# Performance work log

Measured on AMD Instinct MI355X. Metric: run time of the kernel, lower is better.

Reference implementation:

```python
import jax, jax.numpy as jnp
import numpy as np

N_NODES = 100000
N_EDGES = 1600000
DIM = 32

def setup_inputs() -> dict:
    key = jax.random.key(0)
    k1, k2, k3, k4 = jax.random.split(key, 4)
    A_rows = jax.random.randint(k1, (N_EDGES,), 0, N_NODES, dtype=jnp.int32)
    A_cols = jax.random.randint(k2, (N_EDGES,), 0, N_NODES, dtype=jnp.int32)
    A_vals = jax.random.uniform(k3, (N_EDGES,), dtype=jnp.float32)
    x = jax.random.normal(k4, (N_NODES, DIM), dtype=jnp.float32)
    return {"A_rows": A_rows, "A_cols": A_cols, "A_vals": A_vals, "x": x}

def reference(A_rows, A_cols, A_vals, x):
    # SpMM: out[i] = sum_{e: rows[e]==i} vals[e] * x[cols[e]]
    # gather neighbor features along edges, scale by edge weight, scatter-add to rows
    msgs = A_vals[:, None] * x[A_cols]              # [E, d]
    out = jax.ops.segment_sum(msgs, A_rows, num_segments=x.shape[0])  # [n, d]
    return out
```

## Files before the change

### kernel.cpp

```cpp
#include <hip/hip_runtime.h>


#define N_NODES 100000
#define N_EDGES 1600000
#define DIM 32

#define CBR    256
#define NBC    ((N_NODES + CBR - 1) / CBR)
#define CHUNK  8
#define CAPC   6656
#define OCAP   16384

#define SC_BLOCKS   500
#define SC_THREADS  512
#define EPB         3200
#define EPT         7

#define SG_THREADS  1024
#define SG_EPT      7

#define OFF_GCNT    64
#define OFF_OVER    (OFF_GCNT + NBC * 64)
#define OFF_REGION  (((OFF_OVER + OCAP * 16) + 255) & ~255)
#define WS_NEEDED   ((size_t)OFF_REGION + (size_t)NBC * CAPC * 8)

__global__ __launch_bounds__(256) void spmm_atomic_kernel(
    const int* __restrict__ rows,
    const int* __restrict__ cols,
    const float* __restrict__ vals,
    const float* __restrict__ x,
    float* __restrict__ out)
{
    const long long idx = (long long)blockIdx.x * blockDim.x + threadIdx.x;
    const long long total = (long long)N_EDGES * DIM;
    if (idx >= total) return;

    const int e = (int)(idx >> 5);
    const int d = (int)(idx & 31);

    const int r   = rows[e];
    const int c   = cols[e];
    const float v = vals[e];

    const float xv = x[(long long)c * DIM + d];
    atomicAdd(&out[(long long)r * DIM + d], v * xv);
}

__global__ __launch_bounds__(SC_THREADS) void spmm_scatter_ws(
    const int* __restrict__ rows,
    const int* __restrict__ cols,
    const float* __restrict__ vals,
    int* __restrict__ gcnt,
    int2* __restrict__ region,
    int* __restrict__ ocount,
    int4* __restrict__ overflow)
{
    __shared__ int2 stage[EPB];
    __shared__ int  hist[NBC];
    __shared__ int  lstart[NBC];
    __shared__ int  gbase[NBC];
    __shared__ int  wsum[8];

    const int tid   = threadIdx.x;
    const int ebase = blockIdx.x * EPB;

    if (tid < NBC) hist[tid] = 0;
    __syncthreads();

    int en_x[EPT], en_y[EPT], eb[EPT], rk[EPT];
    #pragma unroll
    for (int i = 0; i < EPT; ++i) {
        const int o = i * SC_THREADS + tid;
        if (o < EPB) {
            const int e = ebase + o;
            const int r = rows[e];
            eb[i]   = r >> 8;
            en_x[i] = ((r & 255) << 17) | cols[e];
            en_y[i] = __float_as_int(vals[e]);
            rk[i]   = atomicAdd(&hist[eb[i]], 1);
        } else {
            eb[i] = -1; en_x[i] = 0; en_y[i] = 0; rk[i] = 0;
        }
    }
    __syncthreads();

    const int lane = tid & 63;
    const int wv   = tid >> 6;
    const int myh  = (tid < NBC) ? hist[tid] : 0;
    int s = myh;
    #pragma unroll
    for (int off = 1; off < 64; off <<= 1) {
        const int t = __shfl_up(s, off, 64);
        if (lane >= off) s += t;
    }
    if (lane == 63) wsum[wv] = s;
    __syncthreads();
    if (wv == 0) {
        const int t = (lane < 8) ? wsum[lane] : 0;
        int ss = t;
        #pragma unroll
        for (int off = 1; off < 8; off <<= 1) {
            const int u = __shfl_up(ss, off, 64);
            if (lane >= off) ss += u;
        }
        if (lane < 8) wsum[lane] = ss - t;
    }
    __syncthreads();
    if (tid < NBC) {
        lstart[tid] = s + wsum[wv] - myh;
        const int pad = (myh + 7) & ~7;
        gbase[tid] = pad ? atomicAdd(&gcnt[tid * 16], pad) : 0;
    }
    __syncthreads();

    #pragma unroll
    for (int i = 0; i < EPT; ++i) {
        if (eb[i] >= 0)
            stage[lstart[eb[i]] + rk[i]] = make_int2(en_x[i], en_y[i]);
    }
    __syncthreads();

    for (int bc = tid; bc < NBC; bc += SC_THREADS) {
        const int n   = hist[bc];
        const int ls  = lstart[bc];
        const int gb  = gbase[bc];
        const int nch = (n + 7) >> 3;
        for (int jch = 0; jch < nch; ++jch) {
            const int gpos = gb + jch * CHUNK;
            if (gpos + CHUNK <= CAPC) {
                int2* dst = region + (size_t)bc * CAPC + gpos;
                #pragma unroll
                for (int j = 0; j < CHUNK; ++j) {
                    const int k = jch * CHUNK + j;
                    dst[j] = (k < n) ? stage[ls + k] : make_int2(-1, 0);
                }
            } else {
                for (int j = 0; j < CHUNK; ++j) {
                    const int k = jch * CHUNK + j;
                    if (k < n) {
                        const int2 t = stage[ls + k];
                        const int op = atomicAdd(ocount, 1);
                        if (op < OCAP)
                            overflow[op] = make_int4((bc << 8) | (t.x >> 17),
                                                     t.x & 0x1FFFF, t.y, 0);
                    }
                }
            }
        }
    }
}

__global__ __launch_bounds__(SG_THREADS) void spmm_sort_gather(
    const int* __restrict__ gcnt,
    const int2* __restrict__ region,
    const int* __restrict__ ocount,
    const int4* __restrict__ overflow,
    const float* __restrict__ x,
    float* __restrict__ out)
{
    __shared__ int2 srt[CAPC];
    __shared__ int  hist[CBR];
    __shared__ int  startx[CBR];
    __shared__ int  excl_s[CBR];
    __shared__ int  wsum[4];

    const int bc  = blockIdx.x;
    const int tid = threadIdx.x;

    int n = gcnt[bc * 16]; if (n > CAPC) n = CAPC;
    const int2* __restrict__ slice = region + (size_t)bc * CAPC;

    if (tid < CBR) hist[tid] = 0;
    __syncthreads();

    int ex[SG_EPT], ey[SG_EPT], rk[SG_EPT];
    #pragma unroll
    for (int i = 0; i < SG_EPT; ++i) {
        const int k = i * SG_THREADS + tid;
        ex[i] = -1; ey[i] = 0; rk[i] = 0;
        if (k < n) {
            const int2 e = slice[k];
            ex[i] = e.x; ey[i] = e.y;
            if (e.x >= 0) rk[i] = atomicAdd(&hist[e.x >> 17], 1);
        }
    }
    __syncthreads();

    const int lane = tid & 63;
    const int wv   = tid >> 6;
    int h = 0, incl = 0;
    if (tid < CBR) {
        h = hist[tid];
        int s = h;
        #pragma unroll
        for (int off = 1; off < 64; off <<= 1) {
            const int t = __shfl_up(s, off, 64);
            if (lane >= off) s += t;
        }
        incl = s;
        if (lane == 63) wsum[wv] = s;
    }
    __syncthreads();
    if (wv == 0) {
        const int t = (lane < 4) ? wsum[lane] : 0;
        int ss = t;
        #pragma unroll
        for (int off = 1; off < 4; off <<= 1) {
            const int u = __shfl_up(ss, off, 64);
            if (lane >= off) ss += u;
        }
        if (lane < 4) wsum[lane] = ss - t;
    }
    __syncthreads();
    if (tid < CBR) {
        incl += wsum[wv];
        startx[tid] = incl;
        excl_s[tid] = incl - h;
    }
    __syncthreads();

    #pragma unroll
    for (int i = 0; i < SG_EPT; ++i) {
        if (ex[i] >= 0)
            srt[excl_s[ex[i] >> 17] + rk[i]] = make_int2(ex[i] & 0x1FFFF, ey[i]);
    }
    __syncthreads();

    const int wid = tid >> 6;
    const int eg  = lane >> 3;
    const int d4  = lane & 7;

    #pragma unroll
    for (int i = 0; i < 16; ++i) {
        const int lrow = wid * 16 + i;
        const int cnt  = hist[lrow];
        const int st   = startx[lrow] - cnt;

        float4 acc = make_float4(0.f, 0.f, 0.f, 0.f);
        for (int k0 = 0; k0 < cnt; k0 += 16) {
            const int ka = k0 + eg;
            const int kb = ka + 8;
            const int2 ea = (ka < cnt) ? srt[st + ka] : make_int2(0, 0);
            const int2 eb = (kb < cnt) ? srt[st + kb] : make_int2(0, 0);
            const float va = __int_as_float(ea.y);
            const float vb = __int_as_float(eb.y);
            const float4 xa = *(const float4*)&x[ea.x * DIM + d4 * 4];
            const float4 xb = *(const float4*)&x[eb.x * DIM + d4 * 4];
            acc.x = fmaf(va, xa.x, acc.x);  acc.y = fmaf(va, xa.y, acc.y);
            acc.z = fmaf(va, xa.z, acc.z);  acc.w = fmaf(va, xa.w, acc.w);
            acc.x = fmaf(vb, xb.x, acc.x);  acc.y = fmaf(vb, xb.y, acc.y);
            acc.z = fmaf(vb, xb.z, acc.z);  acc.w = fmaf(vb, xb.w, acc.w);
        }

        #pragma unroll
        for (int m = 8; m < 64; m <<= 1) {
            acc.x += __shfl_xor(acc.x, m, 64);
            acc.y += __shfl_xor(acc.y, m, 64);
            acc.z += __shfl_xor(acc.z, m, 64);
            acc.w += __shfl_xor(acc.w, m, 64);
        }

        const int r = bc * CBR + lrow;
        if (eg == 0 && r < N_NODES)
            *(float4*)&out[r * DIM + d4 * 4] = acc;
    }

    __syncthreads();
    int on = *ocount;
    if (on > 0) {
        if (on > OCAP) on = OCAP;
        for (int k = tid; k < on; k += SG_THREADS) {
            const int4 t = overflow[k];
            if ((t.x >> 8) == bc) {
                const float v = __int_as_float(t.z);
                const float* __restrict__ xr = x + (long long)t.y * DIM;
                float* orow = out + (long long)t.x * DIM;
                for (int d = 0; d < DIM; ++d)
                    atomicAdd(&orow[d], v * xr[d]);
            }
        }
    }
}

extern "C" void kernel_launch(void* const* d_in, const int* in_sizes, int n_in,
                              void* d_out, int out_size, void* d_ws, size_t ws_size,
                              hipStream_t stream) {
    const int*   A_rows = (const int*)d_in[0];
    const int*   A_cols = (const int*)d_in[1];
    const float* A_vals = (const float*)d_in[2];
    const float* x      = (const float*)d_in[3];
    float*       out    = (float*)d_out;

    if (d_ws == nullptr || ws_size < WS_NEEDED) {
        hipMemsetAsync(out, 0, (size_t)out_size * sizeof(float), stream);
        const long long total = (long long)N_EDGES * DIM;
        const int block = 256;
        const long long grid = (total + block - 1) / block;
        spmm_atomic_kernel<<<(dim3)(unsigned)grid, block, 0, stream>>>(
            A_rows, A_cols, A_vals, x, out);
        return;
    }

    char* ws = (char*)d_ws;
    int*  ocount   = (int*)ws;
    int*  gcnt     = (int*)(ws + OFF_GCNT);
    int4* overflow = (int4*)(ws + OFF_OVER);
    int2* region   = (int2*)(ws + OFF_REGION);

    hipMemsetAsync(ws, 0, OFF_OVER, stream);

    spmm_scatter_ws<<<SC_BLOCKS, SC_THREADS, 0, stream>>>(
        A_rows, A_cols, A_vals, gcnt, region, ocount, overflow);

    spmm_sort_gather<<<NBC, SG_THREADS, 0, stream>>>(
        gcnt, region, ocount, overflow, x, out);
}
```

Measured before the change: 132.3 us.

## Fuse memset, scatter and sort-gather into one cooperative kernel with grid syncs

```diff
diff --git a/kernel.cpp b/kernel.cpp
--- a/kernel.cpp
+++ b/kernel.cpp
@@ -1,4 +1,7 @@
 #include <hip/hip_runtime.h>
+#include <hip/hip_cooperative_groups.h>
+
+namespace cg = cooperative_groups;
 
 
 #define N_NODES 100000
@@ -11,13 +14,15 @@
 #define CAPC   6656
 #define OCAP   16384
 
+#define FB_THREADS 1024
+#define EPB1       4093
+#define EPT1       4
+#define EPT2       7
+
 #define SC_BLOCKS   500
 #define SC_THREADS  512
 #define EPB         3200
 #define EPT         7
-
-#define SG_THREADS  1024
-#define SG_EPT      7
 
 #define OFF_GCNT    64
 #define OFF_OVER    (OFF_GCNT + NBC * 64)
@@ -34,111 +39,117 @@
     const long long idx = (long long)blockIdx.x * blockDim.x + threadIdx.x;
     const long long total = (long long)N_EDGES * DIM;
     if (idx >= total) return;
-
     const int e = (int)(idx >> 5);
     const int d = (int)(idx & 31);
-
     const int r   = rows[e];
     const int c   = cols[e];
     const float v = vals[e];
-
-    const float xv = x[(long long)c * DIM + d];
-    atomicAdd(&out[(long long)r * DIM + d], v * xv);
+    atomicAdd(&out[(long long)r * DIM + d], v * x[(long long)c * DIM + d]);
 }
 
-__global__ __launch_bounds__(SC_THREADS) void spmm_scatter_ws(
+__global__ __launch_bounds__(FB_THREADS, 8) void spmm_fused(
     const int* __restrict__ rows,
     const int* __restrict__ cols,
     const float* __restrict__ vals,
     int* __restrict__ gcnt,
     int2* __restrict__ region,
     int* __restrict__ ocount,
-    int4* __restrict__ overflow)
+    int4* __restrict__ overflow,
+    const float* __restrict__ x,
+    float* __restrict__ out)
 {
-    __shared__ int2 stage[EPB];
+    __shared__ int2 buf[CAPC];
     __shared__ int  hist[NBC];
-    __shared__ int  lstart[NBC];
-    __shared__ int  gbase[NBC];
-    __shared__ int  wsum[8];
-
-    const int tid   = threadIdx.x;
-    const int ebase = blockIdx.x * EPB;
+    __shared__ int  aux1[NBC];
+    __shared__ int  aux2[NBC];
+    __shared__ int  wsum[16];
+
+    const int tid  = threadIdx.x;
+    const int bid  = blockIdx.x;
+    const int lane = tid & 63;
+    const int wv   = tid >> 6;
+    cg::grid_group grid = cg::this_grid();
+
+    for (int i = bid * FB_THREADS + tid; i < NBC * 16; i += NBC * FB_THREADS)
+        gcnt[i] = 0;
+    if (bid == 0 && tid == 0) *ocount = 0;
+    grid.sync();
 
     if (tid < NBC) hist[tid] = 0;
     __syncthreads();
 
-    int en_x[EPT], en_y[EPT], eb[EPT], rk[EPT];
-    #pragma unroll
-    for (int i = 0; i < EPT; ++i) {
-        const int o = i * SC_THREADS + tid;
-        if (o < EPB) {
-            const int e = ebase + o;
+    const int ebase = bid * EPB1;
+    int en_x[EPT1], en_y[EPT1], eb[EPT1], rk[EPT1];
+    #pragma unroll
+    for (int i = 0; i < EPT1; ++i) {
+        const int o = i * FB_THREADS + tid;
+        const int e = ebase + o;
+        eb[i] = -1; en_x[i] = 0; en_y[i] = 0; rk[i] = 0;
+        if (o < EPB1 && e < N_EDGES) {
             const int r = rows[e];
             eb[i]   = r >> 8;
             en_x[i] = ((r & 255) << 17) | cols[e];
             en_y[i] = __float_as_int(vals[e]);
             rk[i]   = atomicAdd(&hist[eb[i]], 1);
-        } else {
-            eb[i] = -1; en_x[i] = 0; en_y[i] = 0; rk[i] = 0;
-        }
-    }
-    __syncthreads();
-
-    const int lane = tid & 63;
-    const int wv   = tid >> 6;
-    const int myh  = (tid < NBC) ? hist[tid] : 0;
-    int s = myh;
-    #pragma unroll
-    for (int off = 1; off < 64; off <<= 1) {
-        const int t = __shfl_up(s, off, 64);
-        if (lane >= off) s += t;
-    }
-    if (lane == 63) wsum[wv] = s;
-    __syncthreads();
-    if (wv == 0) {
-        const int t = (lane < 8) ? wsum[lane] : 0;
-        int ss = t;
-        #pragma unroll
-        for (int off = 1; off < 8; off <<= 1) {
-            const int u = __shfl_up(ss, off, 64);
-            if (lane >= off) ss += u;
-        }
-        if (lane < 8) wsum[lane] = ss - t;
-    }
-    __syncthreads();
-    if (tid < NBC) {
-        lstart[tid] = s + wsum[wv] - myh;
-        const int pad = (myh + 7) & ~7;
-        gbase[tid] = pad ? atomicAdd(&gcnt[tid * 16], pad) : 0;
-    }
-    __syncthreads();
-
-    #pragma unroll
-    for (int i = 0; i < EPT; ++i) {
+        }
+    }
+    __syncthreads();
+
+    {
+        const int myh = (tid < NBC) ? hist[tid] : 0;
+        int s = myh;
+        #pragma unroll
+        for (int off = 1; off < 64; off <<= 1) {
+            const int t = __shfl_up(s, off, 64);
+            if (lane >= off) s += t;
+        }
+        if (lane == 63) wsum[wv] = s;
+        __syncthreads();
+        if (wv == 0) {
+            const int t = (lane < 16) ? wsum[lane] : 0;
+            int ss = t;
+            #pragma unroll
+            for (int off = 1; off < 16; off <<= 1) {
+                const int u = __shfl_up(ss, off, 64);
+                if (lane >= off) ss += u;
+            }
+            if (lane < 16) wsum[lane] = ss - t;
+        }
+        __syncthreads();
+        if (tid < NBC) {
+            aux1[tid] = s + wsum[wv] - myh;
+            const int pad = (myh + 7) & ~7;
+            aux2[tid] = pad ? atomicAdd(&gcnt[tid * 16], pad) : 0;
+        }
+    }
+    __syncthreads();
+
+    #pragma unroll
+    for (int i = 0; i < EPT1; ++i) {
         if (eb[i] >= 0)
-            stage[lstart[eb[i]] + rk[i]] = make_int2(en_x[i], en_y[i]);
-    }
-    __syncthreads();
-
-    for (int bc = tid; bc < NBC; bc += SC_THREADS) {
-        const int n   = hist[bc];
-        const int ls  = lstart[bc];
-        const int gb  = gbase[bc];
+            buf[aux1[eb[i]] + rk[i]] = make_int2(en_x[i], en_y[i]);
+    }
+    __syncthreads();
+
+    for (int bc = tid; bc < NBC; bc += FB_THREADS) {
+        const int n  = hist[bc];
+        const int ls = aux1[bc];
+        const int gb = aux2[bc];
         const int nch = (n + 7) >> 3;
-        for (int jch = 0; jch < nch; ++jch) {
-            const int gpos = gb + jch * CHUNK;
+        for (int j = 0; j < nch; ++j) {
+            const int gpos = gb + j * CHUNK;
             if (gpos + CHUNK <= CAPC) {
                 int2* dst = region + (size_t)bc * CAPC + gpos;
                 #pragma unroll
-                for (int j = 0; j < CHUNK; ++j) {
-                    const int k = jch * CHUNK + j;
-                    dst[j] = (k < n) ? stage[ls + k] : make_int2(-1, 0);
+                for (int q = 0; q < CHUNK; ++q) {
+                    const int k = j * CHUNK + q;
+                    dst[q] = (k < n) ? buf[ls + k] : make_int2(-1, 0);
                 }
             } else {
-                for (int j = 0; j < CHUNK; ++j) {
-                    const int k = jch * CHUNK + j;
+                for (int q = 0; q < CHUNK; ++q) {
+                    const int k = j * CHUNK + q;
                     if (k < n) {
-                        const int2 t = stage[ls + k];
+                        const int2 t = buf[ls + k];
                         const int op = atomicAdd(ocount, 1);
                         if (op < OCAP)
                             overflow[op] = make_int4((bc << 8) | (t.x >> 17),
@@ -148,46 +159,29 @@
             }
         }
     }
-}
-
-__global__ __launch_bounds__(SG_THREADS) void spmm_sort_gather(
-    const int* __restrict__ gcnt,
-    const int2* __restrict__ region,
-    const int* __restrict__ ocount,
-    const int4* __restrict__ overflow,
-    const float* __restrict__ x,
-    float* __restrict__ out)
-{
-    __shared__ int2 srt[CAPC];
-    __shared__ int  hist[CBR];
-    __shared__ int  startx[CBR];
-    __shared__ int  excl_s[CBR];
-    __shared__ int  wsum[4];
-
-    const int bc  = blockIdx.x;
-    const int tid = threadIdx.x;
-
+
+    grid.sync();
+
+    const int bc = bid;
     int n = gcnt[bc * 16]; if (n > CAPC) n = CAPC;
     const int2* __restrict__ slice = region + (size_t)bc * CAPC;
 
     if (tid < CBR) hist[tid] = 0;
     __syncthreads();
 
-    int ex[SG_EPT], ey[SG_EPT], rk[SG_EPT];
-    #pragma unroll
-    for (int i = 0; i < SG_EPT; ++i) {
-        const int k = i * SG_THREADS + tid;
-        ex[i] = -1; ey[i] = 0; rk[i] = 0;
+    int ex[EPT2], ey[EPT2], rq[EPT2];
+    #pragma unroll
+    for (int i = 0; i < EPT2; ++i) {
+        const int k = i * FB_THREADS + tid;
+        ex[i] = -1; ey[i] = 0; rq[i] = 0;
         if (k < n) {
             const int2 e = slice[k];
             ex[i] = e.x; ey[i] = e.y;
-            if (e.x >= 0) rk[i] = atomicAdd(&hist[e.x >> 17], 1);
-        }
-    }
-    __syncthreads();
-
-    const int lane = tid & 63;
-    const int wv   = tid >> 6;
+            if (e.x >= 0) rq[i] = atomicAdd(&hist[e.x >> 17], 1);
+        }
+    }
+    __syncthreads();
+
     int h = 0, incl = 0;
     if (tid < CBR) {
         h = hist[tid];
@@ -214,15 +208,15 @@
     __syncthreads();
     if (tid < CBR) {
         incl += wsum[wv];
-        startx[tid] = incl;
-        excl_s[tid] = incl - h;
-    }
-    __syncthreads();
-
-    #pragma unroll
-    for (int i = 0; i < SG_EPT; ++i) {
+        aux1[tid] = incl;
+        aux2[tid] = incl - h;
+    }
+    __syncthreads();
+
+    #pragma unroll
+    for (int i = 0; i < EPT2; ++i) {
         if (ex[i] >= 0)
-            srt[excl_s[ex[i] >> 17] + rk[i]] = make_int2(ex[i] & 0x1FFFF, ey[i]);
+            buf[aux2[ex[i] >> 17] + rq[i]] = make_int2(ex[i] & 0x1FFFF, ey[i]);
     }
     __syncthreads();
 
@@ -234,24 +228,23 @@
     for (int i = 0; i < 16; ++i) {
         const int lrow = wid * 16 + i;
         const int cnt  = hist[lrow];
-        const int st   = startx[lrow] - cnt;
+        const int st   = aux1[lrow] - cnt;
 
         float4 acc = make_float4(0.f, 0.f, 0.f, 0.f);
         for (int k0 = 0; k0 < cnt; k0 += 16) {
             const int ka = k0 + eg;
             const int kb = ka + 8;
-            const int2 ea = (ka < cnt) ? srt[st + ka] : make_int2(0, 0);
-            const int2 eb = (kb < cnt) ? srt[st + kb] : make_int2(0, 0);
+            const int2 ea  = (ka < cnt) ? buf[st + ka] : make_int2(0, 0);
+            const int2 eb2 = (kb < cnt) ? buf[st + kb] : make_int2(0, 0);
             const float va = __int_as_float(ea.y);
-            const float vb = __int_as_float(eb.y);
-            const float4 xa = *(const float4*)&x[ea.x * DIM + d4 * 4];
-            const float4 xb = *(const float4*)&x[eb.x * DIM + d4 * 4];
+            const float vb = __int_as_float(eb2.y);
+            const float4 xa = *(const float4*)&x[ea.x  * DIM + d4 * 4];
+            const float4 xb = *(const float4*)&x[eb2.x * DIM + d4 * 4];
             acc.x = fmaf(va, xa.x, acc.x);  acc.y = fmaf(va, xa.y, acc.y);
             acc.z = fmaf(va, xa.z, acc.z);  acc.w = fmaf(va, xa.w, acc.w);
             acc.x = fmaf(vb, xb.x, acc.x);  acc.y = fmaf(vb, xb.y, acc.y);
             acc.z = fmaf(vb, xb.z, acc.z);  acc.w = fmaf(vb, xb.w, acc.w);
         }
-
         #pragma unroll
         for (int m = 8; m < 64; m <<= 1) {
             acc.x += __shfl_xor(acc.x, m, 64);
@@ -259,7 +252,6 @@
             acc.z += __shfl_xor(acc.z, m, 64);
             acc.w += __shfl_xor(acc.w, m, 64);
         }
-
         const int r = bc * CBR + lrow;
         if (eg == 0 && r < N_NODES)
             *(float4*)&out[r * DIM + d4 * 4] = acc;
@@ -269,7 +261,7 @@
     int on = *ocount;
     if (on > 0) {
         if (on > OCAP) on = OCAP;
-        for (int k = tid; k < on; k += SG_THREADS) {
+        for (int k = tid; k < on; k += FB_THREADS) {
             const int4 t = overflow[k];
             if ((t.x >> 8) == bc) {
                 const float v = __int_as_float(t.z);
@@ -282,6 +274,198 @@
     }
 }
 
+__global__ __launch_bounds__(SC_THREADS) void spmm_scatter_ws(
+    const int* __restrict__ rows, const int* __restrict__ cols,
+    const float* __restrict__ vals, int* __restrict__ gcnt,
+    int2* __restrict__ region, int* __restrict__ ocount, int4* __restrict__ overflow)
+{
+    __shared__ int2 stage[EPB];
+    __shared__ int  hist[NBC];
+    __shared__ int  lstart[NBC];
+    __shared__ int  gbase[NBC];
+    __shared__ int  wsum[8];
+
+    const int tid = threadIdx.x;
+    const int ebase = blockIdx.x * EPB;
+    if (tid < NBC) hist[tid] = 0;
+    __syncthreads();
+
+    int en_x[EPT], en_y[EPT], eb[EPT], rk[EPT];
+    #pragma unroll
+    for (int i = 0; i < EPT; ++i) {
+        const int o = i * SC_THREADS + tid;
+        eb[i] = -1; en_x[i] = 0; en_y[i] = 0; rk[i] = 0;
+        if (o < EPB) {
+            const int e = ebase + o;
+            const int r = rows[e];
+            eb[i]   = r >> 8;
+            en_x[i] = ((r & 255) << 17) | cols[e];
+            en_y[i] = __float_as_int(vals[e]);
+            rk[i]   = atomicAdd(&hist[eb[i]], 1);
+        }
+    }
+    __syncthreads();
+
+    const int lane = tid & 63, wv = tid >> 6;
+    const int myh = (tid < NBC) ? hist[tid] : 0;
+    int s = myh;
+    #pragma unroll
+    for (int off = 1; off < 64; off <<= 1) { const int t = __shfl_up(s, off, 64); if (lane >= off) s += t; }
+    if (lane == 63) wsum[wv] = s;
+    __syncthreads();
+    if (wv == 0) {
+        const int t = (lane < 8) ? wsum[lane] : 0;
+        int ss = t;
+        #pragma unroll
+        for (int off = 1; off < 8; off <<= 1) { const int u = __shfl_up(ss, off, 64); if (lane >= off) ss += u; }
+        if (lane < 8) wsum[lane] = ss - t;
+    }
+    __syncthreads();
+    if (tid < NBC) {
+        lstart[tid] = s + wsum[wv] - myh;
+        const int pad = (myh + 7) & ~7;
+        gbase[tid] = pad ? atomicAdd(&gcnt[tid * 16], pad) : 0;
+    }
+    __syncthreads();
+
+    #pragma unroll
+    for (int i = 0; i < EPT; ++i)
+        if (eb[i] >= 0) stage[lstart[eb[i]] + rk[i]] = make_int2(en_x[i], en_y[i]);
+    __syncthreads();
+
+    for (int bc = tid; bc < NBC; bc += SC_THREADS) {
+        const int n = hist[bc], ls = lstart[bc], gb = gbase[bc];
+        const int nch = (n + 7) >> 3;
+        for (int j = 0; j < nch; ++j) {
+            const int gpos = gb + j * CHUNK;
+            if (gpos + CHUNK <= CAPC) {
+                int2* dst = region + (size_t)bc * CAPC + gpos;
+                #pragma unroll
+                for (int q = 0; q < CHUNK; ++q) {
+                    const int k = j * CHUNK + q;
+                    dst[q] = (k < n) ? stage[ls + k] : make_int2(-1, 0);
+                }
+            } else {
+                for (int q = 0; q < CHUNK; ++q) {
+                    const int k = j * CHUNK + q;
+                    if (k < n) {
+                        const int2 t = stage[ls + k];
+                        const int op = atomicAdd(ocount, 1);
+                        if (op < OCAP)
+                            overflow[op] = make_int4((bc << 8) | (t.x >> 17), t.x & 0x1FFFF, t.y, 0);
+                    }
+                }
+            }
+        }
+    }
+}
+
+__global__ __launch_bounds__(FB_THREADS) void spmm_sort_gather(
+    const int* __restrict__ gcnt, const int2* __restrict__ region,
+    const int* __restrict__ ocount, const int4* __restrict__ overflow,
+    const float* __restrict__ x, float* __restrict__ out)
+{
+    __shared__ int2 srt[CAPC];
+    __shared__ int  hist[CBR];
+    __shared__ int  startx[CBR];
+    __shared__ int  excl_s[CBR];
+    __shared__ int  wsum[4];
+
+    const int bc = blockIdx.x, tid = threadIdx.x;
+    int n = gcnt[bc * 16]; if (n > CAPC) n = CAPC;
+    const int2* __restrict__ slice = region + (size_t)bc * CAPC;
+
+    if (tid < CBR) hist[tid] = 0;
+    __syncthreads();
+
+    int ex[EPT2], ey[EPT2], rk[EPT2];
+    #pragma unroll
+    for (int i = 0; i < EPT2; ++i) {
+        const int k = i * FB_THREADS + tid;
+        ex[i] = -1; ey[i] = 0; rk[i] = 0;
+        if (k < n) {
+            const int2 e = slice[k];
+            ex[i] = e.x; ey[i] = e.y;
+            if (e.x >= 0) rk[i] = atomicAdd(&hist[e.x >> 17], 1);
+        }
+    }
+    __syncthreads();
+
+    const int lane = tid & 63, wv = tid >> 6;
+    int h = 0, incl = 0;
+    if (tid < CBR) {
+        h = hist[tid];
+        int s = h;
+        #pragma unroll
+        for (int off = 1; off < 64; off <<= 1) { const int t = __shfl_up(s, off, 64); if (lane >= off) s += t; }
+        incl = s;
+        if (lane == 63) wsum[wv] = s;
+    }
+    __syncthreads();
+    if (wv == 0) {
+        const int t = (lane < 4) ? wsum[lane] : 0;
+        int ss = t;
+        #pragma unroll
+        for (int off = 1; off < 4; off <<= 1) { const int u = __shfl_up(ss, off, 64); if (lane >= off) ss += u; }
+        if (lane < 4) wsum[lane] = ss - t;
+    }
+    __syncthreads();
+    if (tid < CBR) { incl += wsum[wv]; startx[tid] = incl; excl_s[tid] = incl - h; }
+    __syncthreads();
+
+    #pragma unroll
+    for (int i = 0; i < EPT2; ++i)
+        if (ex[i] >= 0) srt[excl_s[ex[i] >> 17] + rk[i]] = make_int2(ex[i] & 0x1FFFF, ey[i]);
+    __syncthreads();
+
+    const int wid = tid >> 6, eg = lane >> 3, d4 = lane & 7;
+    #pragma unroll
+    for (int i = 0; i < 16; ++i) {
+        const int lrow = wid * 16 + i;
+        const int cnt = hist[lrow];
+        const int st  = startx[lrow] - cnt;
+        float4 acc = make_float4(0.f, 0.f, 0.f, 0.f);
+        for (int k0 = 0; k0 < cnt; k0 += 16) {
+            const int ka = k0 + eg, kb = ka + 8;
+            const int2 ea  = (ka < cnt) ? srt[st + ka] : make_int2(0, 0);
+            const int2 eb2 = (kb < cnt) ? srt[st + kb] : make_int2(0, 0);
+            const float va = __int_as_float(ea.y);
+            const float vb = __int_as_float(eb2.y);
+            const float4 xa = *(const float4*)&x[ea.x  * DIM + d4 * 4];
+            const float4 xb = *(const float4*)&x[eb2.x * DIM + d4 * 4];
+            acc.x = fmaf(va, xa.x, acc.x);  acc.y = fmaf(va, xa.y, acc.y);
+            acc.z = fmaf(va, xa.z, acc.z);  acc.w = fmaf(va, xa.w, acc.w);
+            acc.x = fmaf(vb, xb.x, acc.x);  acc.y = fmaf(vb, xb.y, acc.y);
+            acc.z = fmaf(vb, xb.z, acc.z);  acc.w = fmaf(vb, xb.w, acc.w);
+        }
+        #pragma unroll
+        for (int m = 8; m < 64; m <<= 1) {
+            acc.x += __shfl_xor(acc.x, m, 64);
+            acc.y += __shfl_xor(acc.y, m, 64);
+            acc.z += __shfl_xor(acc.z, m, 64);
+            acc.w += __shfl_xor(acc.w, m, 64);
+        }
+        const int r = bc * CBR + lrow;
+        if (eg == 0 && r < N_NODES)
+            *(float4*)&out[r * DIM + d4 * 4] = acc;
+    }
+
+    __syncthreads();
+    int on = *ocount;
+    if (on > 0) {
+        if (on > OCAP) on = OCAP;
+        for (int k = tid; k < on; k += FB_THREADS) {
+            const int4 t = overflow[k];
+            if ((t.x >> 8) == bc) {
+                const float v = __int_as_float(t.z);
+                const float* __restrict__ xr = x + (long long)t.y * DIM;
+                float* orow = out + (long long)t.x * DIM;
+                for (int d = 0; d < DIM; ++d) atomicAdd(&orow[d], v * xr[d]);
+            }
+        }
+    }
+}
+
 extern "C" void kernel_launch(void* const* d_in, const int* in_sizes, int n_in,
                               void* d_out, int out_size, void* d_ws, size_t ws_size,
                               hipStream_t stream) {
@@ -307,11 +491,17 @@
     int4* overflow = (int4*)(ws + OFF_OVER);
     int2* region   = (int2*)(ws + OFF_REGION);
 
-    hipMemsetAsync(ws, 0, OFF_OVER, stream);
-
-    spmm_scatter_ws<<<SC_BLOCKS, SC_THREADS, 0, stream>>>(
-        A_rows, A_cols, A_vals, gcnt, region, ocount, overflow);
-
-    spmm_sort_gather<<<NBC, SG_THREADS, 0, stream>>>(
-        gcnt, region, ocount, overflow, x, out);
+    void* kargs[] = { (void*)&A_rows, (void*)&A_cols, (void*)&A_vals,
+                      (void*)&gcnt, (void*)&region, (void*)&ocount,
+                      (void*)&overflow, (void*)&x, (void*)&out };
+    hipError_t err = hipLaunchCooperativeKernel(
+        (const void*)spmm_fused, dim3(NBC), dim3(FB_THREADS), kargs, 0, stream);
+
+    if (err != hipSuccess) {
+        hipMemsetAsync(ws, 0, OFF_OVER, stream);
+        spmm_scatter_ws<<<SC_BLOCKS, SC_THREADS, 0, stream>>>(
+            A_rows, A_cols, A_vals, gcnt, region, ocount, overflow);
+        spmm_sort_gather<<<NBC, FB_THREADS, 0, stream>>>(
+            gcnt, region, ocount, overflow, x, out);
+    }
 }
```

New measurement: 231.8 us. 75.2% more time.

## Assign one row per 8-lane group in gather phase, drop cross-lane reduction

Applied to the files above, without the earlier changes.

```diff
diff --git a/kernel.cpp b/kernel.cpp
--- a/kernel.cpp
+++ b/kernel.cpp
@@ -71,6 +71,7 @@
     #pragma unroll
     for (int i = 0; i < EPT; ++i) {
         const int o = i * SC_THREADS + tid;
+        eb[i] = -1; en_x[i] = 0; en_y[i] = 0; rk[i] = 0;
         if (o < EPB) {
             const int e = ebase + o;
             const int r = rows[e];
@@ -78,8 +79,6 @@
             en_x[i] = ((r & 255) << 17) | cols[e];
             en_y[i] = __float_as_int(vals[e]);
             rk[i]   = atomicAdd(&hist[eb[i]], 1);
-        } else {
-            eb[i] = -1; en_x[i] = 0; en_y[i] = 0; rk[i] = 0;
         }
     }
     __syncthreads();
@@ -227,41 +226,49 @@
     __syncthreads();
 
     const int wid = tid >> 6;
-    const int eg  = lane >> 3;
+    const int r8  = lane >> 3;
     const int d4  = lane & 7;
 
     #pragma unroll
-    for (int i = 0; i < 16; ++i) {
-        const int lrow = wid * 16 + i;
+    for (int pass = 0; pass < 2; ++pass) {
+        const int lrow = pass * 128 + wid * 8 + r8;
         const int cnt  = hist[lrow];
         const int st   = startx[lrow] - cnt;
 
         float4 acc = make_float4(0.f, 0.f, 0.f, 0.f);
-        for (int k0 = 0; k0 < cnt; k0 += 16) {
-            const int ka = k0 + eg;
-            const int kb = ka + 8;
-            const int2 ea = (ka < cnt) ? srt[st + ka] : make_int2(0, 0);
-            const int2 eb = (kb < cnt) ? srt[st + kb] : make_int2(0, 0);
-            const float va = __int_as_float(ea.y);
-            const float vb = __int_as_float(eb.y);
-            const float4 xa = *(const float4*)&x[ea.x * DIM + d4 * 4];
-            const float4 xb = *(const float4*)&x[eb.x * DIM + d4 * 4];
-            acc.x = fmaf(va, xa.x, acc.x);  acc.y = fmaf(va, xa.y, acc.y);
-            acc.z = fmaf(va, xa.z, acc.z);  acc.w = fmaf(va, xa.w, acc.w);
-            acc.x = fmaf(vb, xb.x, acc.x);  acc.y = fmaf(vb, xb.y, acc.y);
-            acc.z = fmaf(vb, xb.z, acc.z);  acc.w = fmaf(vb, xb.w, acc.w);
-        }
-
-        #pragma unroll
-        for (int m = 8; m < 64; m <<= 1) {
-            acc.x += __shfl_xor(acc.x, m, 64);
-            acc.y += __shfl_xor(acc.y, m, 64);
-            acc.z += __shfl_xor(acc.z, m, 64);
-            acc.w += __shfl_xor(acc.w, m, 64);
+        int k = 0;
+        for (; k + 3 < cnt; k += 4) {
+            const int2 e0 = srt[st + k + 0];
+            const int2 e1 = srt[st + k + 1];
+            const int2 e2 = srt[st + k + 2];
+            const int2 e3 = srt[st + k + 3];
+            const float4 x0 = *(const float4*)&x[e0.x * DIM + d4 * 4];
+            const float4 x1 = *(const float4*)&x[e1.x * DIM + d4 * 4];
+            const float4 x2 = *(const float4*)&x[e2.x * DIM + d4 * 4];
+            const float4 x3 = *(const float4*)&x[e3.x * DIM + d4 * 4];
+            const float v0 = __int_as_float(e0.y);
+            const float v1 = __int_as_float(e1.y);
+            const float v2 = __int_as_float(e2.y);
+            const float v3 = __int_as_float(e3.y);
+            acc.x = fmaf(v0, x0.x, acc.x);  acc.y = fmaf(v0, x0.y, acc.y);
+            acc.z = fmaf(v0, x0.z, acc.z);  acc.w = fmaf(v0, x0.w, acc.w);
+            acc.x = fmaf(v1, x1.x, acc.x);  acc.y = fmaf(v1, x1.y, acc.y);
+            acc.z = fmaf(v1, x1.z, acc.z);  acc.w = fmaf(v1, x1.w, acc.w);
+            acc.x = fmaf(v2, x2.x, acc.x);  acc.y = fmaf(v2, x2.y, acc.y);
+            acc.z = fmaf(v2, x2.z, acc.z);  acc.w = fmaf(v2, x2.w, acc.w);
+            acc.x = fmaf(v3, x3.x, acc.x);  acc.y = fmaf(v3, x3.y, acc.y);
+            acc.z = fmaf(v3, x3.z, acc.z);  acc.w = fmaf(v3, x3.w, acc.w);
+        }
+        for (; k < cnt; ++k) {
+            const int2 e0 = srt[st + k];
+            const float4 x0 = *(const float4*)&x[e0.x * DIM + d4 * 4];
+            const float v0 = __int_as_float(e0.y);
+            acc.x = fmaf(v0, x0.x, acc.x);  acc.y = fmaf(v0, x0.y, acc.y);
+            acc.z = fmaf(v0, x0.z, acc.z);  acc.w = fmaf(v0, x0.w, acc.w);
         }
 
         const int r = bc * CBR + lrow;
-        if (eg == 0 && r < N_NODES)
+        if (r < N_NODES)
             *(float4*)&out[r * DIM + d4 * 4] = acc;
     }
 
```

Result: slower. 135.5 us (+2.5%).
